# Performance work log

Hardware: AMD Instinct MI355X
Metric: run time of the kernel (lower is better)

## Reference

```python
import jax, jax.numpy as jnp
import numpy as np

N = 50000
E = 800000
D = 128          # in_dim == hidden_dim
EDGE_DIM = 1
H = 128          # hidden_dim


def setup_inputs() -> dict:
    key = jax.random.key(0)
    ks = jax.random.split(key, 16)
    inp = {
        "x": jax.random.normal(ks[0], (N, D), jnp.float32),
        "pos": jax.random.normal(ks[1], (N, 3), jnp.float32),
        "edge_index": jax.random.randint(ks[2], (2, E), 0, N, jnp.int64),
        "edge_attr": jax.random.normal(ks[3], (E, EDGE_DIM), jnp.float32),
        "s": jax.random.uniform(ks[4], (N,), jnp.float32),
    }
    # edge_mlp: Linear(2D+1+edge_dim -> H), SiLU, Linear(H -> H), SiLU
    e_in = 2 * D + 1 + EDGE_DIM
    def lin(k, fan_in, fan_out):
        lim = 1.0 / np.sqrt(fan_in)
        kw, kb = jax.random.split(k)
        W = jax.random.uniform(kw, (fan_in, fan_out), jnp.float32, -lim, lim)
        b = jax.random.uniform(kb, (fan_out,), jnp.float32, -lim, lim)
        return W, b
    inp["W_e1"], inp["b_e1"] = lin(ks[5], e_in, H)
    inp["W_e2"], inp["b_e2"] = lin(ks[6], H, H)
    # node_mlp: Linear(D+H -> H), SiLU, Linear(H -> D)
    inp["W_n1"], inp["b_n1"] = lin(ks[7], D + H, H)
    inp["W_n2"], inp["b_n2"] = lin(ks[8], H, D)
    # coord_mlp: Linear(H -> 1)
    inp["W_c"], inp["b_c"] = lin(ks[9], H, 1)
    return inp


def reference(x, pos, edge_index, edge_attr, s,
              W_e1, b_e1, W_e2, b_e2, W_n1, b_n1, W_n2, b_n2, W_c, b_c):
    src, dst = edge_index[0], edge_index[1]
    n = x.shape[0]

    # edge gather + relative geometry
    diff = pos[dst] - pos[src]                      # [E, 3]
    r2 = jnp.sum(diff * diff, axis=-1, keepdims=True)  # [E, 1]
    e_in = jnp.concatenate([x[dst], x[src], r2, edge_attr], axis=-1)  # [E, 2D+1+edge_dim]

    # edge MLP
    m = jax.nn.silu(e_in @ W_e1 + b_e1)
    m = jax.nn.silu(m @ W_e2 + b_e2)                # [E, H]

    # s-gate on source nodes
    m = m * s[src][:, None]

    # scatter-add aggregation with degree normalization
    m_sum = jax.ops.segment_sum(m, dst, num_segments=n)          # [N, H]
    deg = jax.ops.segment_sum(jnp.ones((m.shape[0], 1), m.dtype), dst, num_segments=n)
    deg = jnp.maximum(deg, 1.0)
    m_sum = m_sum / deg

    # node update
    h = jax.nn.silu(jnp.concatenate([x, m_sum], axis=-1) @ W_n1 + b_n1)
    x_out = h @ W_n2 + b_n2                         # [N, D]

    # coordinate update
    gamma = m @ W_c + b_c                           # [E, 1]
    coord_update = jax.ops.segment_sum(gamma * diff, dst, num_segments=n) / deg
    pos_out = pos + coord_update                    # [N, 3]
    return x_out, pos_out
```

## Files before the change

### kernel.cpp

```cpp
#include <hip/hip_runtime.h>
#include <hip/hip_bf16.h>

#define NN 50000
#define EE 800000
#define SCAN_BLOCKS 196

typedef __bf16 bf16x8_t __attribute__((ext_vector_type(8)));
typedef float f32x4_t __attribute__((ext_vector_type(4)));

__device__ __forceinline__ float silu_f(float v) {
    return v * __builtin_amdgcn_rcpf(1.0f + __expf(-v));
}

__device__ __forceinline__ float bf_lo(unsigned u) { return __uint_as_float(u << 16); }
__device__ __forceinline__ float bf_hi(unsigned u) { return __uint_as_float(u & 0xffff0000u); }

__global__ void prep_kernel(const float* __restrict__ x,
                            const float* __restrict__ We1,
                            const float* __restrict__ We2,
                            const float* __restrict__ Wn1,
                            const float* __restrict__ Wn2,
                            const int* __restrict__ eidx,
                            __bf16* __restrict__ xb,
                            __bf16* __restrict__ WyS,
                            __bf16* __restrict__ We2S,
                            __bf16* __restrict__ Wn1S,
                            __bf16* __restrict__ Wn2S,
                            int* __restrict__ hist) {
    int tid = blockIdx.x * blockDim.x + threadIdx.x;
    int np = gridDim.x * blockDim.x;
    const int NX = NN * 128 / 4;
    for (int i = tid; i < NX; i += np) {
        float4 v = ((const float4*)x)[i];
        __bf16* o = xb + (size_t)i * 4;
        o[0] = (__bf16)v.x; o[1] = (__bf16)v.y; o[2] = (__bf16)v.z; o[3] = (__bf16)v.w;
    }
    for (int i = tid; i < 256 * 128; i += np) {
        int k = i >> 7, n = i & 127;
        int h = (k < 128) ? n : (128 + n);
        int k2 = k & 127;
        WyS[(k2 >> 5) * 8192 + h * 32 + (k2 & 31)] = (__bf16)We1[i];
        Wn1S[(k >> 5) * 4096 + n * 32 + (k & 31)] = (__bf16)Wn1[i];
    }
    for (int i = tid; i < 128 * 128; i += np) {
        int k = i >> 7, n = i & 127;
        We2S[(k >> 5) * 4096 + n * 32 + (k & 31)] = (__bf16)We2[i];
        Wn2S[(k >> 5) * 4096 + n * 32 + (k & 31)] = (__bf16)Wn2[i];
    }
    for (int i = tid; i < EE; i += np) {
        atomicAdd(&hist[eidx[EE + i]], 1);
    }
}

__global__ __launch_bounds__(256, 3)
void ygemm_kernel(const __bf16* __restrict__ xb,
                  const __bf16* __restrict__ WyS,
                  __bf16* __restrict__ ya,
                  __bf16* __restrict__ yb) {
    __shared__ __align__(16) __bf16 Wy[256 * 32];

    const int t = threadIdx.x;
    const int r0 = blockIdx.x * 64;
    const int w = t >> 6;
    const int lane = t & 63;
    const int m_ = lane & 15;
    const int q = lane >> 4;

    const int node = r0 + w * 16 + m_;
    const long nrow = (long)(node < NN ? node : NN - 1) * 128;

    f32x4_t acc[16];
#pragma unroll
    for (int ot = 0; ot < 16; ++ot) acc[ot] = (f32x4_t){0.f, 0.f, 0.f, 0.f};

    const int wrow = t >> 2;
    const int pch = (t & 3) ^ ((wrow >> 1) & 3);
    const int wofs = wrow * 32 + pch * 8;
    const int rofs = m_ * 32 + (q ^ ((m_ >> 1) & 3)) * 8;

    bf16x8_t xf = *(const bf16x8_t*)(xb + nrow + q * 8);
    uint4 v0 = *(const uint4*)(WyS + t * 8);
    uint4 v1 = *(const uint4*)(WyS + 2048 + t * 8);
    uint4 v2 = *(const uint4*)(WyS + 4096 + t * 8);
    uint4 v3 = *(const uint4*)(WyS + 6144 + t * 8);
#pragma unroll
    for (int ks = 0; ks < 4; ++ks) {
        __syncthreads();
        *(uint4*)(Wy + wofs) = v0;
        *(uint4*)(Wy + 64 * 32 + wofs) = v1;
        *(uint4*)(Wy + 128 * 32 + wofs) = v2;
        *(uint4*)(Wy + 192 * 32 + wofs) = v3;
        __syncthreads();
        bf16x8_t nxf;
        if (ks < 3) {
            v0 = *(const uint4*)(WyS + (ks + 1) * 8192 + t * 8);
            v1 = *(const uint4*)(WyS + (ks + 1) * 8192 + 2048 + t * 8);
            v2 = *(const uint4*)(WyS + (ks + 1) * 8192 + 4096 + t * 8);
            v3 = *(const uint4*)(WyS + (ks + 1) * 8192 + 6144 + t * 8);
            nxf = *(const bf16x8_t*)(xb + nrow + (ks + 1) * 32 + q * 8);
        }
#pragma unroll
        for (int ot = 0; ot < 16; ++ot) {
            bf16x8_t wf = *(const bf16x8_t*)(Wy + ot * (16 * 32) + rofs);
            acc[ot] = __builtin_amdgcn_mfma_f32_16x16x32_bf16(wf, xf, acc[ot], 0, 0, 0);
        }
        if (ks < 3) xf = nxf;
    }

    if (node < NN) {
#pragma unroll
        for (int ot = 0; ot < 16; ++ot) {
            union { __bf16 h[4]; uint2 u; } pk;
            pk.h[0] = (__bf16)acc[ot][0];
            pk.h[1] = (__bf16)acc[ot][1];
            pk.h[2] = (__bf16)acc[ot][2];
            pk.h[3] = (__bf16)acc[ot][3];
            int col = (ot & 7) * 16 + q * 4;
            __bf16* dst = (ot < 8 ? ya : yb) + (long)node * 128 + col;
            *(uint2*)dst = pk.u;
        }
    }
}

__global__ void scan_a(const int* __restrict__ hist, int* __restrict__ bsum) {
    __shared__ int sh[256];
    int i = blockIdx.x * 256 + threadIdx.x;
    sh[threadIdx.x] = (i < NN) ? hist[i] : 0;
    __syncthreads();
    for (int s = 128; s > 0; s >>= 1) {
        if (threadIdx.x < s) sh[threadIdx.x] += sh[threadIdx.x + s];
        __syncthreads();
    }
    if (threadIdx.x == 0) bsum[blockIdx.x] = sh[0];
}

__global__ void scan_b(int* __restrict__ bsum) {
    __shared__ int sh[SCAN_BLOCKS];
    int t = threadIdx.x;
    if (t < SCAN_BLOCKS) sh[t] = bsum[t];
    __syncthreads();
    if (t == 0) {
        int acc = 0;
        for (int i = 0; i < SCAN_BLOCKS; ++i) { int v = sh[i]; sh[i] = acc; acc += v; }
    }
    __syncthreads();
    if (t < SCAN_BLOCKS) bsum[t] = sh[t];
}

__global__ void scan_c(const int* __restrict__ hist, const int* __restrict__ bsum,
                       int* __restrict__ off, int* __restrict__ cursor) {
    __shared__ int sh[256];
    int tx = threadIdx.x;
    int i = blockIdx.x * 256 + tx;
    int v = (i < NN) ? hist[i] : 0;
    sh[tx] = v;
    __syncthreads();
    for (int s = 1; s < 256; s <<= 1) {
        int add = (tx >= s) ? sh[tx - s] : 0;
        __syncthreads();
        sh[tx] += add;
        __syncthreads();
    }
    int excl = sh[tx] - v + bsum[blockIdx.x];
    if (i < NN) { off[i] = excl; cursor[i] = excl; }
    if (i == NN - 1) off[NN] = excl + v;
}

__global__ void scatter_kernel(const int* __restrict__ eidx,
                               const float* __restrict__ pos,
                               const float* __restrict__ eattr,
                               const float* __restrict__ s,
                               int* __restrict__ cursor,
                               uint4* __restrict__ erec) {
    int i = blockIdx.x * blockDim.x + threadIdx.x;
    if (i < EE) {
        int si = eidx[i];
        int di = eidx[EE + i];
        int p = atomicAdd(&cursor[di], 1);
        float dx = pos[di * 3 + 0] - pos[si * 3 + 0];
        float dy = pos[di * 3 + 1] - pos[si * 3 + 1];
        float dz = pos[di * 3 + 2] - pos[si * 3 + 2];
        float r2 = dx * dx + dy * dy + dz * dz;
        uint4 a = make_uint4(__float_as_uint(dx), __float_as_uint(dy),
                             __float_as_uint(dz), __float_as_uint(r2));
        uint4 b = make_uint4((unsigned)si, (unsigned)di,
                             __float_as_uint(eattr[i]), __float_as_uint(s[si]));
        erec[(size_t)p * 2] = a;
        erec[(size_t)p * 2 + 1] = b;
    }
}

__global__ __launch_bounds__(256, 3)
void edge_kernel(const __bf16* __restrict__ ya,
                 const __bf16* __restrict__ yb,
                 const uint4* __restrict__ erec,
                 const float* __restrict__ We1,
                 const float* __restrict__ be1,
                 const __bf16* __restrict__ We2S,
                 const float* __restrict__ be2,
                 const float* __restrict__ Wc,
                 const float* __restrict__ bc,
                 float* __restrict__ msum,
                 float* __restrict__ coordsum) {
    __shared__ __align__(16) __bf16 Wt[128 * 32];
    __shared__ __align__(16) __bf16 A2[128 * 136];
    __shared__ __align__(16) float4 s_pk[128];
    __shared__ float s_sg[128], s_g[128];
    __shared__ float s_diff[128 * 3];
    __shared__ int s_dst[128];

    float* Mf = (float*)A2;

    const int t = threadIdx.x;
    const int e0 = blockIdx.x * 128;
    const int w = t >> 6;
    const int lane = t & 63;
    const int m_ = lane & 15;
    const int q = lane >> 4;

    if (t < 128) {
        const uint4* er = erec + (size_t)(e0 + t) * 2;
        uint4 a = er[0];
        uint4 b = er[1];
        s_diff[t * 3 + 0] = __uint_as_float(a.x);
        s_diff[t * 3 + 1] = __uint_as_float(a.y);
        s_diff[t * 3 + 2] = __uint_as_float(a.z);
        s_pk[t] = make_float4(__uint_as_float(a.w), __uint_as_float(b.z),
                              __uint_as_float(b.x), __uint_as_float(b.y));
        s_sg[t] = __uint_as_float(b.w);
        s_dst[t] = (int)b.y;
    }
    __syncthreads();

    const int el0 = w * 16 + m_;
    const int el1 = 64 + w * 16 + m_;

    {
        const int c8 = (t & 15) * 8;
        const int eb = t >> 4;
        float4 b1a = *(const float4*)(be1 + c8);
        float4 b1b = *(const float4*)(be1 + c8 + 4);
        float4 w6a = *(const float4*)(We1 + 256 * 128 + c8);
        float4 w6b = *(const float4*)(We1 + 256 * 128 + c8 + 4);
        float4 w7a = *(const float4*)(We1 + 257 * 128 + c8);
        float4 w7b = *(const float4*)(We1 + 257 * 128 + c8 + 4);
#pragma unroll 4
        for (int i = 0; i < 8; ++i) {
            int e = eb + i * 16;
            float4 pk4 = s_pk[e];
            float r2 = pk4.x, ea = pk4.y;
            int sn = __float_as_int(pk4.z);
            int dn = __float_as_int(pk4.w);
            uint4 av = *(const uint4*)(ya + (long)dn * 128 + c8);
            uint4 bv = *(const uint4*)(yb + (long)sn * 128 + c8);
            union { __bf16 h[8]; uint4 u; } pk;
            pk.h[0] = (__bf16)silu_f(bf_lo(av.x) + bf_lo(bv.x) + b1a.x + r2 * w6a.x + ea * w7a.x);
            pk.h[1] = (__bf16)silu_f(bf_hi(av.x) + bf_hi(bv.x) + b1a.y + r2 * w6a.y + ea * w7a.y);
            pk.h[2] = (__bf16)silu_f(bf_lo(av.y) + bf_lo(bv.y) + b1a.z + r2 * w6a.z + ea * w7a.z);
            pk.h[3] = (__bf16)silu_f(bf_hi(av.y) + bf_hi(bv.y) + b1a.w + r2 * w6a.w + ea * w7a.w);
            pk.h[4] = (__bf16)silu_f(bf_lo(av.z) + bf_lo(bv.z) + b1b.x + r2 * w6b.x + ea * w7b.x);
            pk.h[5] = (__bf16)silu_f(bf_hi(av.z) + bf_hi(bv.z) + b1b.y + r2 * w6b.y + ea * w7b.y);
            pk.h[6] = (__bf16)silu_f(bf_lo(av.w) + bf_lo(bv.w) + b1b.z + r2 * w6b.z + ea * w7b.z);
            pk.h[7] = (__bf16)silu_f(bf_hi(av.w) + bf_hi(bv.w) + b1b.w + r2 * w6b.w + ea * w7b.w);
            *(uint4*)(A2 + e * 136 + c8) = pk.u;
        }
    }

    f32x4_t acc[2][8];
#pragma unroll
    for (int et = 0; et < 2; ++et)
#pragma unroll
        for (int ot = 0; ot < 8; ++ot) acc[et][ot] = (f32x4_t){0.f, 0.f, 0.f, 0.f};

    const int wrow = t >> 2;
    const int pch = (t & 3) ^ ((wrow >> 1) & 3);
    const int wofs = wrow * 32 + pch * 8;
    const int rofs = m_ * 32 + (q ^ ((m_ >> 1) & 3)) * 8;

    uint4 w20 = *(const uint4*)(We2S + t * 8);
    uint4 w21 = *(const uint4*)(We2S + 2048 + t * 8);
#pragma unroll
    for (int ks = 0; ks < 4; ++ks) {
        __syncthreads();
        *(uint4*)(Wt + wofs) = w20;
        *(uint4*)(Wt + 64 * 32 + wofs) = w21;
        __syncthreads();
        if (ks < 3) {
            w20 = *(const uint4*)(We2S + (ks + 1) * 4096 + t * 8);
            w21 = *(const uint4*)(We2S + (ks + 1) * 4096 + 2048 + t * 8);
        }
        bf16x8_t af0 = *(const bf16x8_t*)(A2 + el0 * 136 + ks * 32 + q * 8);
        bf16x8_t af1 = *(const bf16x8_t*)(A2 + el1 * 136 + ks * 32 + q * 8);
#pragma unroll
        for (int ot = 0; ot < 8; ++ot) {
            bf16x8_t wf = *(const bf16x8_t*)(Wt + ot * (16 * 32) + rofs);
            acc[0][ot] = __builtin_amdgcn_mfma_f32_16x16x32_bf16(wf, af0, acc[0][ot], 0, 0, 0);
            acc[1][ot] = __builtin_amdgcn_mfma_f32_16x16x32_bf16(wf, af1, acc[1][ot], 0, 0, 0);
        }
    }

    {
        float sg0 = s_sg[el0], sg1 = s_sg[el1];
        float gp0 = 0.f, gp1 = 0.f;
#pragma unroll
        for (int ot = 0; ot < 8; ++ot) {
            int oc = ot * 16 + q * 4;
            float4 b2 = *(const float4*)(be2 + oc);
            float4 wc = *(const float4*)(Wc + oc);
            f32x4_t v0_ = acc[0][ot], v1_ = acc[1][ot];
            v0_[0] = silu_f(v0_[0] + b2.x) * sg0; v0_[1] = silu_f(v0_[1] + b2.y) * sg0;
            v0_[2] = silu_f(v0_[2] + b2.z) * sg0; v0_[3] = silu_f(v0_[3] + b2.w) * sg0;
            v1_[0] = silu_f(v1_[0] + b2.x) * sg1; v1_[1] = silu_f(v1_[1] + b2.y) * sg1;
            v1_[2] = silu_f(v1_[2] + b2.z) * sg1; v1_[3] = silu_f(v1_[3] + b2.w) * sg1;
            acc[0][ot] = v0_; acc[1][ot] = v1_;
            gp0 += v0_[0] * wc.x + v0_[1] * wc.y + v0_[2] * wc.z + v0_[3] * wc.w;
            gp1 += v1_[0] * wc.x + v1_[1] * wc.y + v1_[2] * wc.z + v1_[3] * wc.w;
        }
        gp0 += __shfl_xor(gp0, 16); gp0 += __shfl_xor(gp0, 32);
        gp1 += __shfl_xor(gp1, 16); gp1 += __shfl_xor(gp1, 32);
        if (q == 0) {
            float b0 = bc[0];
            s_g[el0] = gp0 + b0;
            s_g[el1] = gp1 + b0;
        }
    }
    __syncthreads();

    if (t < 24) {
        int ax = t % 3, ch = t / 3;
        int base = ch * 16;
        float run = 0.f;
        int cur = s_dst[base];
        for (int r = 0; r < 16; ++r) {
            int rr = base + r;
            int d = s_dst[rr];
            if (d != cur) {
                atomicAdd(&coordsum[cur * 3 + ax], run);
                run = 0.f; cur = d;
            }
            run += s_g[rr] * s_diff[rr * 3 + ax];
        }
        atomicAdd(&coordsum[cur * 3 + ax], run);
    }

#pragma unroll
    for (int ph = 0; ph < 2; ++ph) {
        int lr = w * 16 + m_;
#pragma unroll
        for (int ot = 0; ot < 8; ++ot)
            *(f32x4_t*)(Mf + lr * 132 + ot * 16 + q * 4) = acc[ph][ot];
        __syncthreads();
        {
            int c = t & 127;
            int half = t >> 7;
            int base = ph * 64 + half * 32;
            float run = 0.f;
            int cur = s_dst[base];
            for (int r = 0; r < 32; ++r) {
                int d = s_dst[base + r];
                if (d != cur) {
                    atomicAdd(&msum[(long)cur * 128 + c], run);
                    run = 0.f; cur = d;
                }
                run += Mf[(half * 32 + r) * 132 + c];
            }
            atomicAdd(&msum[(long)cur * 128 + c], run);
        }
        __syncthreads();
    }
}

__global__ __launch_bounds__(256, 4)
void node_kernel(const __bf16* __restrict__ xb,
                 const float* __restrict__ msum,
                 const int* __restrict__ off,
                 const __bf16* __restrict__ Wn1S,
                 const float* __restrict__ bn1,
                 const __bf16* __restrict__ Wn2S,
                 const float* __restrict__ bn2,
                 const float* __restrict__ pos,
                 const float* __restrict__ csum,
                 float* __restrict__ xout,
                 float* __restrict__ pout) {
    __shared__ __align__(16) __bf16 Wt[128 * 32];
    __shared__ __align__(16) __bf16 A2[64 * 136];

    const int t = threadIdx.x;
    const int r0 = blockIdx.x * 64;
    const int w = t >> 6;
    const int lane = t & 63;
    const int m_ = lane & 15;
    const int q = lane >> 4;

    if (t < 192) {
        int node = r0 + t / 3;
        if (node < NN) {
            int dg = off[node + 1] - off[node];
            float inv = 1.f / (float)(dg < 1 ? 1 : dg);
            int fl = node * 3 + t % 3;
            pout[fl] = pos[fl] + csum[fl] * inv;
        }
    }

    const int node = r0 + w * 16 + m_;
    const int ncl = node < NN ? node : NN - 1;
    const long nrow = (long)ncl * 128;
    const int dg = off[ncl + 1] - off[ncl];
    const float inv = 1.f / (float)(dg < 1 ? 1 : dg);

    f32x4_t acc[8];
#pragma unroll
    for (int ot = 0; ot < 8; ++ot) acc[ot] = (f32x4_t){0.f, 0.f, 0.f, 0.f};

    const int wrow = t >> 2;
    const int pch = (t & 3) ^ ((wrow >> 1) & 3);
    const int wofs = wrow * 32 + pch * 8;
    const int rofs = m_ * 32 + (q ^ ((m_ >> 1) & 3)) * 8;

    bf16x8_t xf = *(const bf16x8_t*)(xb + nrow + q * 8);
    float4 mf0, mf1;
    uint4 v0 = *(const uint4*)(Wn1S + t * 8);
    uint4 v1 = *(const uint4*)(Wn1S + 2048 + t * 8);
#pragma unroll
    for (int ks = 0; ks < 8; ++ks) {
        __syncthreads();
        *(uint4*)(Wt + wofs) = v0;
        *(uint4*)(Wt + 64 * 32 + wofs) = v1;
        __syncthreads();
        bf16x8_t nxf; float4 nm0, nm1;
        if (ks < 7) {
            v0 = *(const uint4*)(Wn1S + (ks + 1) * 4096 + t * 8);
            v1 = *(const uint4*)(Wn1S + (ks + 1) * 4096 + 2048 + t * 8);
            if (ks + 1 < 4) {
                nxf = *(const bf16x8_t*)(xb + nrow + (ks + 1) * 32 + q * 8);
            } else {
                const float* mp = msum + nrow + (ks + 1 - 4) * 32 + q * 8;
                nm0 = *(const float4*)(mp);
                nm1 = *(const float4*)(mp + 4);
            }
        }
        bf16x8_t cf;
        if (ks < 4) {
            cf = xf;
        } else {
            union { __bf16 h[8]; bf16x8_t v; } u;
            u.h[0] = (__bf16)(mf0.x * inv); u.h[1] = (__bf16)(mf0.y * inv);
            u.h[2] = (__bf16)(mf0.z * inv); u.h[3] = (__bf16)(mf0.w * inv);
            u.h[4] = (__bf16)(mf1.x * inv); u.h[5] = (__bf16)(mf1.y * inv);
            u.h[6] = (__bf16)(mf1.z * inv); u.h[7] = (__bf16)(mf1.w * inv);
            cf = u.v;
        }
#pragma unroll
        for (int ot = 0; ot < 8; ++ot) {
            bf16x8_t wf = *(const bf16x8_t*)(Wt + ot * (16 * 32) + rofs);
            acc[ot] = __builtin_amdgcn_mfma_f32_16x16x32_bf16(wf, cf, acc[ot], 0, 0, 0);
        }
        if (ks < 7) {
            if (ks + 1 < 4) xf = nxf;
            else { mf0 = nm0; mf1 = nm1; }
        }
    }

#pragma unroll
    for (int ot = 0; ot < 8; ++ot) {
        float4 b1 = *(const float4*)(bn1 + ot * 16 + q * 4);
        union { __bf16 h[4]; uint2 u; } pk;
        pk.h[0] = (__bf16)silu_f(acc[ot][0] + b1.x);
        pk.h[1] = (__bf16)silu_f(acc[ot][1] + b1.y);
        pk.h[2] = (__bf16)silu_f(acc[ot][2] + b1.z);
        pk.h[3] = (__bf16)silu_f(acc[ot][3] + b1.w);
        *(uint2*)(A2 + (w * 16 + m_) * 136 + ot * 16 + q * 4) = pk.u;
        acc[ot] = (f32x4_t){0.f, 0.f, 0.f, 0.f};
    }

    uint4 u0 = *(const uint4*)(Wn2S + t * 8);
    uint4 u1 = *(const uint4*)(Wn2S + 2048 + t * 8);
#pragma unroll
    for (int ks = 0; ks < 4; ++ks) {
        __syncthreads();
        *(uint4*)(Wt + wofs) = u0;
        *(uint4*)(Wt + 64 * 32 + wofs) = u1;
        __syncthreads();
        if (ks < 3) {
            u0 = *(const uint4*)(Wn2S + (ks + 1) * 4096 + t * 8);
            u1 = *(const uint4*)(Wn2S + (ks + 1) * 4096 + 2048 + t * 8);
        }
        bf16x8_t af = *(const bf16x8_t*)(A2 + (w * 16 + m_) * 136 + ks * 32 + q * 8);
#pragma unroll
        for (int ot = 0; ot < 8; ++ot) {
            bf16x8_t wf = *(const bf16x8_t*)(Wt + ot * (16 * 32) + rofs);
            acc[ot] = __builtin_amdgcn_mfma_f32_16x16x32_bf16(wf, af, acc[ot], 0, 0, 0);
        }
    }

    if (node < NN) {
#pragma unroll
        for (int ot = 0; ot < 8; ++ot) {
            float4 b2 = *(const float4*)(bn2 + ot * 16 + q * 4);
            float4 o;
            o.x = acc[ot][0] + b2.x; o.y = acc[ot][1] + b2.y;
            o.z = acc[ot][2] + b2.z; o.w = acc[ot][3] + b2.w;
            *(float4*)(xout + nrow + ot * 16 + q * 4) = o;
        }
    }
}

extern "C" void kernel_launch(void* const* d_in, const int* in_sizes, int n_in,
                              void* d_out, int out_size, void* d_ws, size_t ws_size,
                              hipStream_t stream) {
    const float* x     = (const float*)d_in[0];
    const float* pos   = (const float*)d_in[1];
    const int*   eidx  = (const int*)d_in[2];
    const float* eattr = (const float*)d_in[3];
    const float* s     = (const float*)d_in[4];
    const float* We1   = (const float*)d_in[5];
    const float* be1   = (const float*)d_in[6];
    const float* We2   = (const float*)d_in[7];
    const float* be2   = (const float*)d_in[8];
    const float* Wn1   = (const float*)d_in[9];
    const float* bn1   = (const float*)d_in[10];
    const float* Wn2   = (const float*)d_in[11];
    const float* bn2   = (const float*)d_in[12];
    const float* Wc    = (const float*)d_in[13];
    const float* bc    = (const float*)d_in[14];

    char* ws = (char*)d_ws;
    __bf16* xb     = (__bf16*)(ws);
    __bf16* WyS    = (__bf16*)(ws + 12800000);
    __bf16* We2S   = (__bf16*)(ws + 12865536);
    __bf16* Wn1S   = (__bf16*)(ws + 12898304);
    __bf16* Wn2S   = (__bf16*)(ws + 12963840);
    float*  msum   = (float*)(ws + 12996608);
    float*  csum   = (float*)(ws + 38596608);
    int*    hist   = (int*)(ws + 39196608);
    int*    off    = (int*)(ws + 39396608);
    int*    cursor = (int*)(ws + 39596672);
    uint4*  erec   = (uint4*)(ws + 39796736);
    int*    bsum   = (int*)(ws + 65396736);
    __bf16* ya     = (__bf16*)(ws + 65397760);
    __bf16* yb     = (__bf16*)(ws + 78197760);

    float* xout = (float*)d_out;
    float* pout = xout + (size_t)NN * 128;

    hipMemsetAsync(ws + 12996608, 0, 26400000, stream);
    prep_kernel<<<1024, 256, 0, stream>>>(x, We1, We2, Wn1, Wn2, eidx,
                                          xb, WyS, We2S, Wn1S, Wn2S, hist);
    ygemm_kernel<<<(NN + 63) / 64, 256, 0, stream>>>(xb, WyS, ya, yb);
    scan_a<<<SCAN_BLOCKS, 256, 0, stream>>>(hist, bsum);
    scan_b<<<1, 256, 0, stream>>>(bsum);
    scan_c<<<SCAN_BLOCKS, 256, 0, stream>>>(hist, bsum, off, cursor);
    scatter_kernel<<<(EE + 255) / 256, 256, 0, stream>>>(eidx, pos, eattr, s, cursor, erec);
    edge_kernel<<<EE / 128, 256, 0, stream>>>(ya, yb, erec,
                                              We1, be1, We2S, be2, Wc, bc,
                                              msum, csum);
    node_kernel<<<(NN + 63) / 64, 256, 0, stream>>>(xb, msum, off, Wn1S, bn1, Wn2S, bn2,
                                                    pos, csum, xout, pout);
}
```

Baseline: 348.7 us.

## Remap edge blocks per XCD, fold first-layer bias into y GEMM, vectorize bf16 conversion

Edge blocks are remapped so each XCD processes a contiguous range of dst-sorted edges, improving L2 locality for gathered node rows. The first-layer bias is added in the node-level y GEMM instead of per edge. The edge kernel now reads edge records directly from global memory rather than staging them in shared memory, which drops a barrier but adds redundant per-thread loads. The x to bf16 conversion now writes 16-byte vectors. Rounding the bias into the bf16 y values slightly changes numerics.

Result: no change. 349.5 us (+0.2%).

```diff
diff --git a/kernel.cpp b/kernel.cpp
--- a/kernel.cpp
+++ b/kernel.cpp
@@ -29,11 +29,16 @@
                             int* __restrict__ hist) {
     int tid = blockIdx.x * blockDim.x + threadIdx.x;
     int np = gridDim.x * blockDim.x;
-    const int NX = NN * 128 / 4;
-    for (int i = tid; i < NX; i += np) {
-        float4 v = ((const float4*)x)[i];
-        __bf16* o = xb + (size_t)i * 4;
-        o[0] = (__bf16)v.x; o[1] = (__bf16)v.y; o[2] = (__bf16)v.z; o[3] = (__bf16)v.w;
+    const int NX8 = NN * 16;
+    for (int i = tid; i < NX8; i += np) {
+        float4 v0 = ((const float4*)x)[(size_t)i * 2];
+        float4 v1 = ((const float4*)x)[(size_t)i * 2 + 1];
+        union { __bf16 h[8]; uint4 u; } pk;
+        pk.h[0] = (__bf16)v0.x; pk.h[1] = (__bf16)v0.y;
+        pk.h[2] = (__bf16)v0.z; pk.h[3] = (__bf16)v0.w;
+        pk.h[4] = (__bf16)v1.x; pk.h[5] = (__bf16)v1.y;
+        pk.h[6] = (__bf16)v1.z; pk.h[7] = (__bf16)v1.w;
+        ((uint4*)xb)[i] = pk.u;
     }
     for (int i = tid; i < 256 * 128; i += np) {
         int k = i >> 7, n = i & 127;
@@ -55,6 +60,7 @@
 __global__ __launch_bounds__(256, 3)
 void ygemm_kernel(const __bf16* __restrict__ xb,
                   const __bf16* __restrict__ WyS,
+                  const float* __restrict__ be1,
                   __bf16* __restrict__ ya,
                   __bf16* __restrict__ yb) {
     __shared__ __align__(16) __bf16 Wy[256 * 32];
@@ -110,12 +116,14 @@
     if (node < NN) {
 #pragma unroll
         for (int ot = 0; ot < 16; ++ot) {
+            int col = (ot & 7) * 16 + q * 4;
+            float4 b1 = make_float4(0.f, 0.f, 0.f, 0.f);
+            if (ot < 8) b1 = *(const float4*)(be1 + col);
             union { __bf16 h[4]; uint2 u; } pk;
-            pk.h[0] = (__bf16)acc[ot][0];
-            pk.h[1] = (__bf16)acc[ot][1];
-            pk.h[2] = (__bf16)acc[ot][2];
-            pk.h[3] = (__bf16)acc[ot][3];
-            int col = (ot & 7) * 16 + q * 4;
+            pk.h[0] = (__bf16)(acc[ot][0] + b1.x);
+            pk.h[1] = (__bf16)(acc[ot][1] + b1.y);
+            pk.h[2] = (__bf16)(acc[ot][2] + b1.z);
+            pk.h[3] = (__bf16)(acc[ot][3] + b1.w);
             __bf16* dst = (ot < 8 ? ya : yb) + (long)node * 128 + col;
             *(uint2*)dst = pk.u;
         }
@@ -195,7 +203,6 @@
                  const __bf16* __restrict__ yb,
                  const uint4* __restrict__ erec,
                  const float* __restrict__ We1,
-                 const float* __restrict__ be1,
                  const __bf16* __restrict__ We2S,
                  const float* __restrict__ be2,
                  const float* __restrict__ Wc,
@@ -204,7 +211,6 @@
                  float* __restrict__ coordsum) {
     __shared__ __align__(16) __bf16 Wt[128 * 32];
     __shared__ __align__(16) __bf16 A2[128 * 136];
-    __shared__ __align__(16) float4 s_pk[128];
     __shared__ float s_sg[128], s_g[128];
     __shared__ float s_diff[128 * 3];
     __shared__ int s_dst[128];
@@ -212,7 +218,11 @@
     float* Mf = (float*)A2;
 
     const int t = threadIdx.x;
-    const int e0 = blockIdx.x * 128;
+    const int bid = blockIdx.x;
+    const int xcd = bid & 7;
+    const int idx = bid >> 3;
+    const int wgid = (xcd < 2) ? xcd * 782 + idx : 2 * 782 + (xcd - 2) * 781 + idx;
+    const int e0 = wgid * 128;
     const int w = t >> 6;
     const int lane = t & 63;
     const int m_ = lane & 15;
@@ -225,12 +235,9 @@
         s_diff[t * 3 + 0] = __uint_as_float(a.x);
         s_diff[t * 3 + 1] = __uint_as_float(a.y);
         s_diff[t * 3 + 2] = __uint_as_float(a.z);
-        s_pk[t] = make_float4(__uint_as_float(a.w), __uint_as_float(b.z),
-                              __uint_as_float(b.x), __uint_as_float(b.y));
         s_sg[t] = __uint_as_float(b.w);
         s_dst[t] = (int)b.y;
     }
-    __syncthreads();
 
     const int el0 = w * 16 + m_;
     const int el1 = 64 + w * 16 + m_;
@@ -238,30 +245,32 @@
     {
         const int c8 = (t & 15) * 8;
         const int eb = t >> 4;
-        float4 b1a = *(const float4*)(be1 + c8);
-        float4 b1b = *(const float4*)(be1 + c8 + 4);
         float4 w6a = *(const float4*)(We1 + 256 * 128 + c8);
         float4 w6b = *(const float4*)(We1 + 256 * 128 + c8 + 4);
         float4 w7a = *(const float4*)(We1 + 257 * 128 + c8);
         float4 w7b = *(const float4*)(We1 + 257 * 128 + c8 + 4);
+        const float* erf = (const float*)erec;
 #pragma unroll 4
         for (int i = 0; i < 8; ++i) {
             int e = eb + i * 16;
-            float4 pk4 = s_pk[e];
-            float r2 = pk4.x, ea = pk4.y;
-            int sn = __float_as_int(pk4.z);
-            int dn = __float_as_int(pk4.w);
+            size_t eo = (size_t)(e0 + e) * 8;
+            float r2 = erf[eo + 3];
+            uint4 bb = *(const uint4*)(erf + eo + 4);
+            int sn = (int)bb.x;
+            int dn = (int)bb.y;
+            float ea = __uint_as_float(bb.z);
             uint4 av = *(const uint4*)(ya + (long)dn * 128 + c8);
             uint4 bv = *(const uint4*)(yb + (long)sn * 128 + c8);
             union { __bf16 h[8]; uint4 u; } pk;
-            pk.h[0] = (__bf16)silu_f(bf_lo(av.x) + bf_lo(bv.x) + b1a.x + r2 * w6a.x + ea * w7a.x);
-            pk.h[1] = (__bf16)silu_f(bf_hi(av.x) + bf_hi(bv.x) + b1a.y + r2 * w6a.y + ea * w7a.y);
-            pk.h[2] = (__bf16)silu_f(bf_lo(av.y) + bf_lo(bv.y) + b1a.z + r2 * w6a.z + ea * w7a.z);
-            pk.h[3] = (__bf16)silu_f(bf_hi(av.y) + bf_hi(bv.y) + b1a.w + r2 * w6a.w + ea * w7a.w);
-            pk.h[4] = (__bf16)silu_f(bf_lo(av.z) + bf_lo(bv.z) + b1b.x + r2 * w6b.x + ea * w7b.x);
-            pk.h[5] = (__bf16)silu_f(bf_hi(av.z) + bf_hi(bv.z) + b1b.y + r2 * w6b.y + ea * w7b.y);
-            pk.h[6] = (__bf16)silu_f(bf_lo(av.w) + bf_lo(bv.w) + b1b.z + r2 * w6b.z + ea * w7b.z);
-            pk.h[7] = (__bf16)silu_f(bf_hi(av.w) + bf_hi(bv.w) + b1b.w + r2 * w6b.w + ea * w7b.w);
+            float s0, s1;
+            s0 = bf_lo(av.x) + bf_lo(bv.x); pk.h[0] = (__bf16)silu_f(s0 + r2 * w6a.x + ea * w7a.x);
+            s1 = bf_hi(av.x) + bf_hi(bv.x); pk.h[1] = (__bf16)silu_f(s1 + r2 * w6a.y + ea * w7a.y);
+            s0 = bf_lo(av.y) + bf_lo(bv.y); pk.h[2] = (__bf16)silu_f(s0 + r2 * w6a.z + ea * w7a.z);
+            s1 = bf_hi(av.y) + bf_hi(bv.y); pk.h[3] = (__bf16)silu_f(s1 + r2 * w6a.w + ea * w7a.w);
+            s0 = bf_lo(av.z) + bf_lo(bv.z); pk.h[4] = (__bf16)silu_f(s0 + r2 * w6b.x + ea * w7b.x);
+            s1 = bf_hi(av.z) + bf_hi(bv.z); pk.h[5] = (__bf16)silu_f(s1 + r2 * w6b.y + ea * w7b.y);
+            s0 = bf_lo(av.w) + bf_lo(bv.w); pk.h[6] = (__bf16)silu_f(s0 + r2 * w6b.z + ea * w7b.z);
+            s1 = bf_hi(av.w) + bf_hi(bv.w); pk.h[7] = (__bf16)silu_f(s1 + r2 * w6b.w + ea * w7b.w);
             *(uint4*)(A2 + e * 136 + c8) = pk.u;
         }
     }
@@ -546,13 +555,13 @@
     hipMemsetAsync(ws + 12996608, 0, 26400000, stream);
     prep_kernel<<<1024, 256, 0, stream>>>(x, We1, We2, Wn1, Wn2, eidx,
                                           xb, WyS, We2S, Wn1S, Wn2S, hist);
-    ygemm_kernel<<<(NN + 63) / 64, 256, 0, stream>>>(xb, WyS, ya, yb);
+    ygemm_kernel<<<(NN + 63) / 64, 256, 0, stream>>>(xb, WyS, be1, ya, yb);
     scan_a<<<SCAN_BLOCKS, 256, 0, stream>>>(hist, bsum);
     scan_b<<<1, 256, 0, stream>>>(bsum);
     scan_c<<<SCAN_BLOCKS, 256, 0, stream>>>(hist, bsum, off, cursor);
     scatter_kernel<<<(EE + 255) / 256, 256, 0, stream>>>(eidx, pos, eattr, s, cursor, erec);
     edge_kernel<<<EE / 128, 256, 0, stream>>>(ya, yb, erec,
-                                              We1, be1, We2S, be2, Wc, bc,
+                                              We1, We2S, be2, Wc, bc,
                                               msum, csum);
     node_kernel<<<(NN + 63) / 64, 256, 0, stream>>>(xb, msum, off, Wn1S, bn1, Wn2S, bn2,
                                                     pos, csum, xout, pout);
```
